# Performance work log

Hardware: AMD Instinct MI355X
Metric: run time of the kernel (lower is better)

Reference implementation:

```python
import jax, jax.numpy as jnp
import numpy as np

N_NODES = 65536
N_EDGES = 1048576


def gcn_conv(x, W, b, src, dst, n_nodes):
    """PyG GCNConv (normalize=True, add_self_loops already applied in src/dst):
    out = D^{-1/2} (A+I) D^{-1/2} X W + b, aggregated at dst (target) nodes."""
    deg = jax.ops.segment_sum(jnp.ones_like(dst, dtype=x.dtype), dst, num_segments=n_nodes)
    dis = jax.lax.rsqrt(jnp.maximum(deg, 1.0))  # self loops guarantee deg >= 1
    norm = dis[src] * dis[dst]                  # [E]
    h = x @ W                                   # [N, out]
    agg = jax.ops.segment_sum(h[src] * norm[:, None], dst, num_segments=n_nodes)
    return agg + b


def setup_inputs() -> dict:
    key = jax.random.key(0)
    ks = jax.random.split(key, 8)
    x = jax.random.normal(ks[0], (N_NODES, 128), dtype=jnp.float32)
    edge_index = jax.random.randint(ks[1], (2, N_EDGES), 0, N_NODES, dtype=jnp.int64)
    dims = [(128, 256), (256, 128), (128, 64)]
    params = {}
    for i, (din, dout) in enumerate(dims):
        scale = 1.0 / np.sqrt(din)
        params[f"W{i+1}"] = jax.random.uniform(ks[2 + i], (din, dout), dtype=jnp.float32, minval=-scale, maxval=scale)
        params[f"b{i+1}"] = jnp.zeros((dout,), dtype=jnp.float32)
    return {"x": x, "edge_index": edge_index, **params}


def reference(x, edge_index, W1, b1, W2, b2, W3, b3):
    n = x.shape[0]
    loop = jnp.arange(n, dtype=edge_index.dtype)
    src = jnp.concatenate([edge_index[0], loop])  # add self loops
    dst = jnp.concatenate([edge_index[1], loop])
    for W, b in ((W1, b1), (W2, b2), (W3, b3)):
        x = gcn_conv(x, W, b, src, dst, n)
        x = jax.nn.softmax(jax.nn.relu(x), axis=1)  # ReLU then Softmax(dim=1) per layer
    return x
```

## Files before the change

### kernel.cpp

```cpp
#include <hip/hip_runtime.h>
#include <cstdint>
#include <cstddef>

#define N_NODES 65536
#define N_EDGES 1048576
#define E_TOT   (N_EDGES + N_NODES)
#define CAP     5120

using short8  = __attribute__((ext_vector_type(8))) short;
using floatx4 = __attribute__((ext_vector_type(4))) float;
using half8   = __attribute__((ext_vector_type(8))) _Float16;
using half4   = __attribute__((ext_vector_type(4))) _Float16;
typedef unsigned short ushort_t;

__device__ inline void split_bf16(float a, short& hi, short& lo) {
    unsigned u  = __float_as_uint(a);
    unsigned hr = (u + 0x7fffu + ((u >> 16) & 1u)) >> 16;
    float    hf = __uint_as_float(hr << 16);
    hi = (short)hr;
    float    lf = a - hf;
    lo = (short)(__float_as_uint(lf) >> 16);
}


__global__ __launch_bounds__(1024) void k_bucket(const int* __restrict__ src, const int* __restrict__ dst,
                                                 int* __restrict__ gcur, unsigned* __restrict__ pk) {
    __shared__ int cnt[256];
    __shared__ int cur[256];
    int tid = threadIdx.x;
    if (tid < 256) cnt[tid] = 0;
    __syncthreads();
    int base = blockIdx.x * 4096;
    #pragma unroll
    for (int j = 0; j < 4; ++j) {
        int d = __builtin_nontemporal_load(&dst[base + j * 1024 + tid]);
        atomicAdd(&cnt[d >> 8], 1);
    }
    __syncthreads();
    if (tid < 256) cur[tid] = CAP * tid + atomicAdd(&gcur[tid], cnt[tid]);
    __syncthreads();
    #pragma unroll
    for (int j = 0; j < 4; ++j) {
        int e = base + j * 1024 + tid;
        int d = __builtin_nontemporal_load(&dst[e]);
        int s = __builtin_nontemporal_load(&src[e]);
        int pos = atomicAdd(&cur[d >> 8], 1);
        pk[pos] = ((unsigned)s << 16) | (unsigned)d;
    }
}

__global__ __launch_bounds__(256) void k_boff(const int* __restrict__ gcur, int* __restrict__ boff,
                                              int* __restrict__ off) {
    __shared__ int sb[256];
    int tid = threadIdx.x;
    int v = gcur[tid] + 256;
    sb[tid] = v;
    __syncthreads();
    #pragma unroll
    for (int s = 1; s < 256; s <<= 1) {
        int t = (tid >= s) ? sb[tid - s] : 0;
        __syncthreads();
        sb[tid] += t;
        __syncthreads();
    }
    boff[tid] = sb[tid] - v;
    if (tid == 255) boff[256] = sb[255];
    if (tid == 0) off[N_NODES] = E_TOT;
}

__global__ __launch_bounds__(1024) void k_sortb(const unsigned* __restrict__ pk, const int* __restrict__ gcur,
                                                const int* __restrict__ boff, int* __restrict__ off,
                                                float* __restrict__ dis, ushort_t* __restrict__ ssort) {
    __shared__ int cnt[256];
    __shared__ int sb[256];
    __shared__ int cur[256];
    int b = blockIdx.x;
    int tid = threadIdx.x;
    int n = gcur[b];
    const unsigned* p = pk + (size_t)b * CAP;
    if (tid < 256) cnt[tid] = 0;
    __syncthreads();
    for (int i = tid; i < n; i += 1024) atomicAdd(&cnt[p[i] & 255u], 1);
    __syncthreads();
    if (tid < 256) sb[tid] = cnt[tid];
    __syncthreads();
    #pragma unroll
    for (int s = 1; s < 256; s <<= 1) {
        int t = (tid < 256 && tid >= s) ? sb[tid - s] : 0;
        __syncthreads();
        if (tid < 256) sb[tid] += t;
        __syncthreads();
    }
    if (tid < 256) {
        int deg = cnt[tid];
        int o = boff[b] + (sb[tid] - deg) + tid;
        int d = b * 256 + tid;
        off[d] = o;
        dis[d] = rsqrtf((float)(deg + 1));
        ssort[o + deg] = (ushort_t)d;
        cur[tid] = o;
    }
    __syncthreads();
    for (int i = tid; i < n; i += 1024) {
        unsigned v = p[i];
        int pos = atomicAdd(&cur[v & 255u], 1);
        ssort[pos] = (ushort_t)(v >> 16);
    }
}


#define G1 (16 * 4 * 64)
#define G2 (8 * 8 * 64)
#define G3 (4 * 4 * 64)
#define NBX 8192
#define NBW ((G1 + G2 + G3 + 255) / 256)

__device__ inline void convw_split(const float* W, int K, int N, short* Bh, short* Bl, int g) {
    int lane = g & 63;
    int kt = (g >> 6) % (K / 32);
    int nt = (g >> 6) / (K / 32);
    int n = nt * 16 + (lane & 15);
    int kbase = kt * 32 + (lane >> 4) * 8;
    #pragma unroll
    for (int j = 0; j < 8; ++j) {
        short h, l;
        split_bf16(W[(size_t)(kbase + j) * N + n], h, l);
        Bh[(size_t)g * 8 + j] = h;
        Bl[(size_t)g * 8 + j] = l;
    }
}

__device__ inline void convw_h(const float* W, int K, int N, _Float16* Bf, int g) {
    int lane = g & 63;
    int kt = (g >> 6) % (K / 32);
    int nt = (g >> 6) / (K / 32);
    int n = nt * 16 + (lane & 15);
    int kbase = kt * 32 + (lane >> 4) * 8;
    #pragma unroll
    for (int j = 0; j < 8; ++j)
        Bf[(size_t)g * 8 + j] = (_Float16)W[(size_t)(kbase + j) * N + n];
}

__global__ __launch_bounds__(256) void k_fused(
        const float* __restrict__ x, const float* __restrict__ dis, _Float16* __restrict__ xh,
        const float* __restrict__ W1, short* __restrict__ w1h, short* __restrict__ w1l,
        const float* __restrict__ W2, _Float16* __restrict__ w2f,
        const float* __restrict__ W3, _Float16* __restrict__ w3f) {
    int b = blockIdx.x;
    if (b < NBX) {
        int idx = (b * 256 + threadIdx.x) * 4;
        int row = idx >> 7;
        float d = dis[row];
        float4 v = *(const float4*)(x + idx);
        half4 o = {(_Float16)(d * v.x), (_Float16)(d * v.y), (_Float16)(d * v.z), (_Float16)(d * v.w)};
        *(half4*)(xh + idx) = o;
    } else {
        int g = (b - NBX) * 256 + threadIdx.x;
        if (g < G1)                 convw_split(W1, 128, 256, w1h, w1l, g);
        else if (g < G1 + G2)       convw_h(W2, 256, 128, w2f, g - G1);
        else if (g < G1 + G2 + G3)  convw_h(W3, 128, 64, w3f, g - G1 - G2);
    }
}


template <int K, int N>
__global__ __launch_bounds__(256) void k_mms(const _Float16* __restrict__ A,
                                             const short* __restrict__ Bh, const short* __restrict__ Bl,
                                             const float* __restrict__ bias, _Float16* __restrict__ Cout) {
    constexpr int NT = N / 16;
    constexpr int KT = K / 32;
    int tid = threadIdx.x;
    int wave = tid >> 6, lane = tid & 63;
    int quad = lane >> 4, col = lane & 15;
    size_t row0 = (size_t)blockIdx.x * 64;
    const _Float16* ap = A + (row0 + wave * 16 + col) * K + quad * 8;

    floatx4 acc[NT];
    #pragma unroll
    for (int t = 0; t < NT; ++t) acc[t] = (floatx4)0.0f;

    for (int kt = 0; kt < KT; ++kt) {
        half8 a8 = *(const half8*)(ap + kt * 32);
        short ah[8], al[8];
        #pragma unroll
        for (int j = 0; j < 8; ++j) split_bf16((float)a8[j], ah[j], al[j]);
        short8 afh = *(short8*)ah;
        short8 afl = *(short8*)al;
        #pragma unroll
        for (int nt = 0; nt < NT; ++nt) {
            size_t bi = ((size_t)(nt * KT + kt) * 64 + lane);
            short8 bfh = ((const short8*)Bh)[bi];
            short8 bfl = ((const short8*)Bl)[bi];
            acc[nt] = __builtin_amdgcn_mfma_f32_16x16x32_bf16(afh, bfh, acc[nt], 0, 0, 0);
            acc[nt] = __builtin_amdgcn_mfma_f32_16x16x32_bf16(afh, bfl, acc[nt], 0, 0, 0);
            acc[nt] = __builtin_amdgcn_mfma_f32_16x16x32_bf16(afl, bfh, acc[nt], 0, 0, 0);
        }
    }

    size_t rbase = row0 + wave * 16 + quad * 4;
    float bv[NT];
    #pragma unroll
    for (int nt = 0; nt < NT; ++nt) bv[nt] = bias[nt * 16 + col];
    float mr[4] = {0.f, 0.f, 0.f, 0.f};
    #pragma unroll
    for (int nt = 0; nt < NT; ++nt)
        #pragma unroll
        for (int r = 0; r < 4; ++r) {
            float v = fmaxf(acc[nt][r] + bv[nt], 0.0f);
            acc[nt][r] = v;
            mr[r] = fmaxf(mr[r], v);
        }
    #pragma unroll
    for (int mask = 1; mask < 16; mask <<= 1)
        #pragma unroll
        for (int r = 0; r < 4; ++r) mr[r] = fmaxf(mr[r], __shfl_xor(mr[r], mask, 64));
    float sr[4] = {0.f, 0.f, 0.f, 0.f};
    #pragma unroll
    for (int nt = 0; nt < NT; ++nt)
        #pragma unroll
        for (int r = 0; r < 4; ++r) {
            float t = __expf(acc[nt][r] - mr[r]);
            acc[nt][r] = t;
            sr[r] += t;
        }
    #pragma unroll
    for (int mask = 1; mask < 16; mask <<= 1)
        #pragma unroll
        for (int r = 0; r < 4; ++r) sr[r] += __shfl_xor(sr[r], mask, 64);
    float inv[4];
    #pragma unroll
    for (int r = 0; r < 4; ++r) inv[r] = 1.0f / sr[r];
    #pragma unroll
    for (int nt = 0; nt < NT; ++nt)
        #pragma unroll
        for (int r = 0; r < 4; ++r)
            Cout[(rbase + r) * N + nt * 16 + col] = (_Float16)(acc[nt][r] * inv[r]);
}


template <int K, int N>
__global__ __launch_bounds__(256) void k_mmh(const _Float16* __restrict__ A,
                                             const _Float16* __restrict__ Bf,
                                             const float* __restrict__ dis, _Float16* __restrict__ Cout) {
    constexpr int NT = N / 16;
    constexpr int KT = K / 32;
    int tid = threadIdx.x;
    int wave = tid >> 6, lane = tid & 63;
    int quad = lane >> 4, col = lane & 15;
    size_t row0 = (size_t)blockIdx.x * 64;
    const _Float16* ap = A + (row0 + wave * 16 + col) * K + quad * 8;

    floatx4 acc[NT];
    #pragma unroll
    for (int t = 0; t < NT; ++t) acc[t] = (floatx4)0.0f;

    for (int kt = 0; kt < KT; ++kt) {
        half8 a8 = *(const half8*)(ap + kt * 32);
        #pragma unroll
        for (int nt = 0; nt < NT; ++nt) {
            half8 bf = ((const half8*)Bf)[(size_t)(nt * KT + kt) * 64 + lane];
            acc[nt] = __builtin_amdgcn_mfma_f32_16x16x32_f16(a8, bf, acc[nt], 0, 0, 0);
        }
    }

    size_t rbase = row0 + wave * 16 + quad * 4;
    float4 d4 = *(const float4*)(dis + rbase);
    float dr[4] = {d4.x, d4.y, d4.z, d4.w};
    #pragma unroll
    for (int nt = 0; nt < NT; ++nt)
        #pragma unroll
        for (int r = 0; r < 4; ++r)
            Cout[(rbase + r) * N + nt * 16 + col] = (_Float16)(acc[nt][r] * dr[r]);
}


template <bool ACT>
__global__ __launch_bounds__(256) void k_agg128h(const _Float16* __restrict__ h, const int* __restrict__ off,
                                                 const ushort_t* __restrict__ ss, const float* __restrict__ dis,
                                                 const float* __restrict__ bias, _Float16* __restrict__ out) {
    int lane = threadIdx.x & 63;
    int sub = lane >> 4;
    int li  = lane & 15;
    int c0  = li * 8;
    int n = blockIdx.x * 4 + (threadIdx.x >> 6);
    int e0 = off[n], e1 = off[n + 1];
    int e = e0;
    float acc[8];
    #pragma unroll
    for (int j = 0; j < 8; ++j) acc[j] = 0.0f;

    if (ACT) {
        half8 hacc = {0, 0, 0, 0, 0, 0, 0, 0};
        for (; e + 16 <= e1; e += 16) {
            int s0 = ss[e + sub];
            int s1 = ss[e + 4 + sub];
            int s2 = ss[e + 8 + sub];
            int s3 = ss[e + 12 + sub];
            half8 v0 = *(const half8*)(h + (size_t)s0 * 128 + c0);
            half8 v1 = *(const half8*)(h + (size_t)s1 * 128 + c0);
            half8 v2 = *(const half8*)(h + (size_t)s2 * 128 + c0);
            half8 v3 = *(const half8*)(h + (size_t)s3 * 128 + c0);
            hacc += (v0 + v1) + (v2 + v3);
        }
        for (; e + 8 <= e1; e += 8) {
            int sa = ss[e + sub];
            int sb = ss[e + 4 + sub];
            half8 va = *(const half8*)(h + (size_t)sa * 128 + c0);
            half8 vb = *(const half8*)(h + (size_t)sb * 128 + c0);
            hacc += va + vb;
        }
        #pragma unroll
        for (int j = 0; j < 8; ++j) acc[j] = (float)hacc[j];
    } else {
        for (; e + 16 <= e1; e += 16) {
            int s0 = ss[e + sub];
            int s1 = ss[e + 4 + sub];
            int s2 = ss[e + 8 + sub];
            int s3 = ss[e + 12 + sub];
            half8 v0 = *(const half8*)(h + (size_t)s0 * 128 + c0);
            half8 v1 = *(const half8*)(h + (size_t)s1 * 128 + c0);
            half8 v2 = *(const half8*)(h + (size_t)s2 * 128 + c0);
            half8 v3 = *(const half8*)(h + (size_t)s3 * 128 + c0);
            half8 vs = (v0 + v1) + (v2 + v3);
            #pragma unroll
            for (int j = 0; j < 8; ++j) acc[j] += (float)vs[j];
        }
        for (; e + 8 <= e1; e += 8) {
            int sa = ss[e + sub];
            int sb = ss[e + 4 + sub];
            half8 va = *(const half8*)(h + (size_t)sa * 128 + c0);
            half8 vb = *(const half8*)(h + (size_t)sb * 128 + c0);
            half8 vs = va + vb;
            #pragma unroll
            for (int j = 0; j < 8; ++j) acc[j] += (float)vs[j];
        }
    }
    while (e < e1) {
        int rem = e1 - e;
        int idx = e + sub;
        if (idx >= e1) idx = e1 - 1;
        int s = ss[idx];
        half8 v = *(const half8*)(h + (size_t)s * 128 + c0);
        float w = (sub < rem) ? 1.0f : 0.0f;
        #pragma unroll
        for (int j = 0; j < 8; ++j) acc[j] = fmaf(w, (float)v[j], acc[j]);
        e += 4;
    }

    #pragma unroll
    for (int mask = 32; mask >= 16; mask >>= 1)
        #pragma unroll
        for (int j = 0; j < 8; ++j) acc[j] += __shfl_xor(acc[j], mask, 64);

    float dn = dis[n];
    if (ACT) {
        float m = 0.0f;
        #pragma unroll
        for (int j = 0; j < 8; ++j) {
            float v = fmaxf(fmaf(acc[j], dn, bias[c0 + j]), 0.0f);
            acc[j] = v;
            m = fmaxf(m, v);
        }
        #pragma unroll
        for (int mask = 8; mask > 0; mask >>= 1) m = fmaxf(m, __shfl_xor(m, mask, 64));
        float sum = 0.0f;
        #pragma unroll
        for (int j = 0; j < 8; ++j) {
            float t = __expf(acc[j] - m);
            acc[j] = t;
            sum += t;
        }
        #pragma unroll
        for (int mask = 8; mask > 0; mask >>= 1) sum += __shfl_xor(sum, mask, 64);
        float inv = 1.0f / sum;
        #pragma unroll
        for (int j = 0; j < 8; ++j) acc[j] *= inv;
    } else {
        #pragma unroll
        for (int j = 0; j < 8; ++j) acc[j] *= dn;
    }
    if (sub == 0) {
        half8 o;
        #pragma unroll
        for (int j = 0; j < 8; ++j) o[j] = (_Float16)acc[j];
        *(half8*)(out + (size_t)n * 128 + c0) = o;
    }
}


__global__ __launch_bounds__(256) void k_agg64h(const _Float16* __restrict__ h, const int* __restrict__ off,
                                                const ushort_t* __restrict__ ss, const float* __restrict__ dis,
                                                const float* __restrict__ bias, float* __restrict__ out) {
    int lane = threadIdx.x & 63;
    int sub = lane >> 3;
    int li  = lane & 7;
    int c0  = li * 8;
    int n = blockIdx.x * 4 + (threadIdx.x >> 6);
    int e0 = off[n], e1 = off[n + 1];
    int e = e0;
    float acc[8];
    #pragma unroll
    for (int j = 0; j < 8; ++j) acc[j] = 0.0f;

    half8 hacc = {0, 0, 0, 0, 0, 0, 0, 0};
    for (; e + 16 <= e1; e += 16) {
        int s0 = ss[e + sub];
        int s1 = ss[e + 8 + sub];
        half8 v0 = *(const half8*)(h + (size_t)s0 * 64 + c0);
        half8 v1 = *(const half8*)(h + (size_t)s1 * 64 + c0);
        hacc += v0 + v1;
    }
    for (; e + 8 <= e1; e += 8) {
        int s = ss[e + sub];
        half8 v = *(const half8*)(h + (size_t)s * 64 + c0);
        hacc += v;
    }
    #pragma unroll
    for (int j = 0; j < 8; ++j) acc[j] = (float)hacc[j];

    int rem = e1 - e;
    if (rem > 0) {
        int idx = e + sub;
        if (idx >= e1) idx = e1 - 1;
        int s = ss[idx];
        half8 v = *(const half8*)(h + (size_t)s * 64 + c0);
        float w = (sub < rem) ? 1.0f : 0.0f;
        #pragma unroll
        for (int j = 0; j < 8; ++j) acc[j] = fmaf(w, (float)v[j], acc[j]);
    }

    #pragma unroll
    for (int mask = 32; mask >= 8; mask >>= 1)
        #pragma unroll
        for (int j = 0; j < 8; ++j) acc[j] += __shfl_xor(acc[j], mask, 64);

    float dn = dis[n];
    float m = 0.0f;
    #pragma unroll
    for (int j = 0; j < 8; ++j) {
        float v = fmaxf(fmaf(acc[j], dn, bias[c0 + j]), 0.0f);
        acc[j] = v;
        m = fmaxf(m, v);
    }
    #pragma unroll
    for (int mask = 4; mask > 0; mask >>= 1) m = fmaxf(m, __shfl_xor(m, mask, 64));
    float sum = 0.0f;
    #pragma unroll
    for (int j = 0; j < 8; ++j) {
        float t = __expf(acc[j] - m);
        acc[j] = t;
        sum += t;
    }
    #pragma unroll
    for (int mask = 4; mask > 0; mask >>= 1) sum += __shfl_xor(sum, mask, 64);
    float inv = 1.0f / sum;
    if (sub == 0) {
        float* op = out + (size_t)n * 64 + c0;
        *(float4*)(op)     = make_float4(acc[0] * inv, acc[1] * inv, acc[2] * inv, acc[3] * inv);
        *(float4*)(op + 4) = make_float4(acc[4] * inv, acc[5] * inv, acc[6] * inv, acc[7] * inv);
    }
}


extern "C" void kernel_launch(void* const* d_in, const int* in_sizes, int n_in,
                              void* d_out, int out_size, void* d_ws, size_t ws_size,
                              hipStream_t stream) {
    const float* x  = (const float*)d_in[0];
    const int*   ei = (const int*)d_in[1];
    const float* W1 = (const float*)d_in[2];
    const float* b1 = (const float*)d_in[3];
    const float* W2 = (const float*)d_in[4];
    const float* b2 = (const float*)d_in[5];
    const float* W3 = (const float*)d_in[6];
    const float* b3 = (const float*)d_in[7];
    const int* srcE = ei;
    const int* dstE = ei + N_EDGES;

    char* p = (char*)d_ws;
    auto carve = [&](size_t bytes) {
        char* q = p;
        p += (bytes + 255) & ~(size_t)255;
        return q;
    };
    int*          gcur  = (int*)carve(sizeof(int) * 256);
    int*          boff  = (int*)carve(sizeof(int) * 257);
    int*          off   = (int*)carve(sizeof(int) * (N_NODES + 1));
    float*        dis   = (float*)carve(sizeof(float) * N_NODES);
    unsigned*     pk    = (unsigned*)carve(sizeof(unsigned) * 256 * CAP);
    ushort_t*     ssort = (ushort_t*)carve(sizeof(ushort_t) * E_TOT);
    short*        w1h   = (short*)carve(sizeof(short) * 128 * 256);
    short*        w1l   = (short*)carve(sizeof(short) * 128 * 256);
    _Float16*     w2f   = (_Float16*)carve(sizeof(_Float16) * 256 * 128);
    _Float16*     w3f   = (_Float16*)carve(sizeof(_Float16) * 128 * 64);
    _Float16*     xh    = (_Float16*)carve(sizeof(_Float16) * (size_t)N_NODES * 128);
    _Float16*     a0h   = (_Float16*)carve(sizeof(_Float16) * (size_t)N_NODES * 128);
    _Float16*     x1h   = (_Float16*)carve(sizeof(_Float16) * (size_t)N_NODES * 256);
    _Float16*     x2h   = (_Float16*)carve(sizeof(_Float16) * (size_t)N_NODES * 128);
    _Float16*     hh    = (_Float16*)carve(sizeof(_Float16) * (size_t)N_NODES * 128);

    (void)hipMemsetAsync(gcur, 0, sizeof(int) * 256, stream);
    k_bucket<<<256, 1024, 0, stream>>>(srcE, dstE, gcur, pk);
    k_boff<<<1, 256, 0, stream>>>(gcur, boff, off);
    k_sortb<<<256, 1024, 0, stream>>>(pk, gcur, boff, off, dis, ssort);
    k_fused<<<NBX + NBW, 256, 0, stream>>>(x, dis, xh, W1, w1h, w1l, W2, w2f, W3, w3f);

    k_agg128h<false><<<N_NODES / 4, 256, 0, stream>>>(xh, off, ssort, dis, nullptr, a0h);
    k_mms<128, 256><<<N_NODES / 64, 256, 0, stream>>>(a0h, w1h, w1l, b1, x1h);
    k_mmh<256, 128><<<N_NODES / 64, 256, 0, stream>>>(x1h, w2f, dis, hh);
    k_agg128h<true><<<N_NODES / 4, 256, 0, stream>>>(hh, off, ssort, dis, b2, x2h);
    k_mmh<128, 64><<<N_NODES / 64, 256, 0, stream>>>(x2h, w3f, dis, hh);
    k_agg64h<<<N_NODES / 4, 256, 0, stream>>>(hh, off, ssort, dis, b3, (float*)d_out);
}
```

Measured before the change: 292.8 us.

## Assign multiple nodes per wavefront in aggregation kernels instead of one

```diff
diff --git a/kernel.cpp b/kernel.cpp
--- a/kernel.cpp
+++ b/kernel.cpp
@@ -274,190 +274,105 @@
 }
 
 
-template <bool ACT>
-__global__ __launch_bounds__(256) void k_agg128h(const _Float16* __restrict__ h, const int* __restrict__ off,
-                                                 const ushort_t* __restrict__ ss, const float* __restrict__ dis,
-                                                 const float* __restrict__ bias, _Float16* __restrict__ out) {
+template <int LPN, bool ACT, typename OutT>
+__global__ __launch_bounds__(256) void k_aggq(const _Float16* __restrict__ h, const int* __restrict__ off,
+                                              const ushort_t* __restrict__ ss, const float* __restrict__ dis,
+                                              const float* __restrict__ bias, OutT* __restrict__ out) {
+    constexpr int D = LPN * 8;
+    constexpr int NPW = 64 / LPN;
     int lane = threadIdx.x & 63;
-    int sub = lane >> 4;
-    int li  = lane & 15;
-    int c0  = li * 8;
-    int n = blockIdx.x * 4 + (threadIdx.x >> 6);
+    int grp  = lane / LPN;
+    int li   = lane & (LPN - 1);
+    int c0   = li * 8;
+    int n = (blockIdx.x * 4 + (threadIdx.x >> 6)) * NPW + grp;
     int e0 = off[n], e1 = off[n + 1];
+
+    const _Float16* hb = h + c0;
+
+    half8 hacc = {0, 0, 0, 0, 0, 0, 0, 0};
+    float facc[8];
+    #pragma unroll
+    for (int j = 0; j < 8; ++j) facc[j] = 0.0f;
+
     int e = e0;
-    float acc[8];
-    #pragma unroll
-    for (int j = 0; j < 8; ++j) acc[j] = 0.0f;
-
-    if (ACT) {
-        half8 hacc = {0, 0, 0, 0, 0, 0, 0, 0};
-        for (; e + 16 <= e1; e += 16) {
-            int s0 = ss[e + sub];
-            int s1 = ss[e + 4 + sub];
-            int s2 = ss[e + 8 + sub];
-            int s3 = ss[e + 12 + sub];
-            half8 v0 = *(const half8*)(h + (size_t)s0 * 128 + c0);
-            half8 v1 = *(const half8*)(h + (size_t)s1 * 128 + c0);
-            half8 v2 = *(const half8*)(h + (size_t)s2 * 128 + c0);
-            half8 v3 = *(const half8*)(h + (size_t)s3 * 128 + c0);
-            hacc += (v0 + v1) + (v2 + v3);
-        }
-        for (; e + 8 <= e1; e += 8) {
-            int sa = ss[e + sub];
-            int sb = ss[e + 4 + sub];
-            half8 va = *(const half8*)(h + (size_t)sa * 128 + c0);
-            half8 vb = *(const half8*)(h + (size_t)sb * 128 + c0);
-            hacc += va + vb;
-        }
-        #pragma unroll
-        for (int j = 0; j < 8; ++j) acc[j] = (float)hacc[j];
-    } else {
-        for (; e + 16 <= e1; e += 16) {
-            int s0 = ss[e + sub];
-            int s1 = ss[e + 4 + sub];
-            int s2 = ss[e + 8 + sub];
-            int s3 = ss[e + 12 + sub];
-            half8 v0 = *(const half8*)(h + (size_t)s0 * 128 + c0);
-            half8 v1 = *(const half8*)(h + (size_t)s1 * 128 + c0);
-            half8 v2 = *(const half8*)(h + (size_t)s2 * 128 + c0);
-            half8 v3 = *(const half8*)(h + (size_t)s3 * 128 + c0);
-            half8 vs = (v0 + v1) + (v2 + v3);
+    for (; e + 4 <= e1; e += 4) {
+        int s0 = ss[e];
+        int s1 = ss[e + 1];
+        int s2 = ss[e + 2];
+        int s3 = ss[e + 3];
+        half8 v0 = *(const half8*)(hb + (size_t)s0 * D);
+        half8 v1 = *(const half8*)(hb + (size_t)s1 * D);
+        half8 v2 = *(const half8*)(hb + (size_t)s2 * D);
+        half8 v3 = *(const half8*)(hb + (size_t)s3 * D);
+        half8 p = (v0 + v1) + (v2 + v3);
+        if constexpr (ACT) {
+            hacc += p;
+        } else {
             #pragma unroll
-            for (int j = 0; j < 8; ++j) acc[j] += (float)vs[j];
-        }
-        for (; e + 8 <= e1; e += 8) {
-            int sa = ss[e + sub];
-            int sb = ss[e + 4 + sub];
-            half8 va = *(const half8*)(h + (size_t)sa * 128 + c0);
-            half8 vb = *(const half8*)(h + (size_t)sb * 128 + c0);
-            half8 vs = va + vb;
-            #pragma unroll
-            for (int j = 0; j < 8; ++j) acc[j] += (float)vs[j];
-        }
-    }
-    while (e < e1) {
-        int rem = e1 - e;
-        int idx = e + sub;
-        if (idx >= e1) idx = e1 - 1;
-        int s = ss[idx];
-        half8 v = *(const half8*)(h + (size_t)s * 128 + c0);
-        float w = (sub < rem) ? 1.0f : 0.0f;
-        #pragma unroll
-        for (int j = 0; j < 8; ++j) acc[j] = fmaf(w, (float)v[j], acc[j]);
-        e += 4;
-    }
-
-    #pragma unroll
-    for (int mask = 32; mask >= 16; mask >>= 1)
-        #pragma unroll
-        for (int j = 0; j < 8; ++j) acc[j] += __shfl_xor(acc[j], mask, 64);
-
-    float dn = dis[n];
-    if (ACT) {
-        float m = 0.0f;
-        #pragma unroll
-        for (int j = 0; j < 8; ++j) {
-            float v = fmaxf(fmaf(acc[j], dn, bias[c0 + j]), 0.0f);
-            acc[j] = v;
-            m = fmaxf(m, v);
-        }
-        #pragma unroll
-        for (int mask = 8; mask > 0; mask >>= 1) m = fmaxf(m, __shfl_xor(m, mask, 64));
-        float sum = 0.0f;
-        #pragma unroll
-        for (int j = 0; j < 8; ++j) {
-            float t = __expf(acc[j] - m);
-            acc[j] = t;
-            sum += t;
-        }
-        #pragma unroll
-        for (int mask = 8; mask > 0; mask >>= 1) sum += __shfl_xor(sum, mask, 64);
-        float inv = 1.0f / sum;
-        #pragma unroll
-        for (int j = 0; j < 8; ++j) acc[j] *= inv;
-    } else {
-        #pragma unroll
-        for (int j = 0; j < 8; ++j) acc[j] *= dn;
-    }
-    if (sub == 0) {
-        half8 o;
-        #pragma unroll
-        for (int j = 0; j < 8; ++j) o[j] = (_Float16)acc[j];
-        *(half8*)(out + (size_t)n * 128 + c0) = o;
-    }
-}
-
-
-__global__ __launch_bounds__(256) void k_agg64h(const _Float16* __restrict__ h, const int* __restrict__ off,
-                                                const ushort_t* __restrict__ ss, const float* __restrict__ dis,
-                                                const float* __restrict__ bias, float* __restrict__ out) {
-    int lane = threadIdx.x & 63;
-    int sub = lane >> 3;
-    int li  = lane & 7;
-    int c0  = li * 8;
-    int n = blockIdx.x * 4 + (threadIdx.x >> 6);
-    int e0 = off[n], e1 = off[n + 1];
-    int e = e0;
-    float acc[8];
-    #pragma unroll
-    for (int j = 0; j < 8; ++j) acc[j] = 0.0f;
-
-    half8 hacc = {0, 0, 0, 0, 0, 0, 0, 0};
-    for (; e + 16 <= e1; e += 16) {
-        int s0 = ss[e + sub];
-        int s1 = ss[e + 8 + sub];
-        half8 v0 = *(const half8*)(h + (size_t)s0 * 64 + c0);
-        half8 v1 = *(const half8*)(h + (size_t)s1 * 64 + c0);
-        hacc += v0 + v1;
-    }
-    for (; e + 8 <= e1; e += 8) {
-        int s = ss[e + sub];
-        half8 v = *(const half8*)(h + (size_t)s * 64 + c0);
-        hacc += v;
-    }
-    #pragma unroll
-    for (int j = 0; j < 8; ++j) acc[j] = (float)hacc[j];
-
+            for (int j = 0; j < 8; ++j) facc[j] += (float)p[j];
+        }
+    }
     int rem = e1 - e;
     if (rem > 0) {
-        int idx = e + sub;
-        if (idx >= e1) idx = e1 - 1;
-        int s = ss[idx];
-        half8 v = *(const half8*)(h + (size_t)s * 64 + c0);
-        float w = (sub < rem) ? 1.0f : 0.0f;
-        #pragma unroll
-        for (int j = 0; j < 8; ++j) acc[j] = fmaf(w, (float)v[j], acc[j]);
-    }
-
-    #pragma unroll
-    for (int mask = 32; mask >= 8; mask >>= 1)
-        #pragma unroll
-        for (int j = 0; j < 8; ++j) acc[j] += __shfl_xor(acc[j], mask, 64);
+        int s0 = ss[e];
+        half8 p = *(const half8*)(hb + (size_t)s0 * D);
+        if (rem > 1) {
+            int s1 = ss[e + 1];
+            p += *(const half8*)(hb + (size_t)s1 * D);
+        }
+        if (rem > 2) {
+            int s2 = ss[e + 2];
+            p += *(const half8*)(hb + (size_t)s2 * D);
+        }
+        if constexpr (ACT) {
+            hacc += p;
+        } else {
+            #pragma unroll
+            for (int j = 0; j < 8; ++j) facc[j] += (float)p[j];
+        }
+    }
+    if constexpr (ACT) {
+        #pragma unroll
+        for (int j = 0; j < 8; ++j) facc[j] = (float)hacc[j];
+    }
 
     float dn = dis[n];
-    float m = 0.0f;
-    #pragma unroll
-    for (int j = 0; j < 8; ++j) {
-        float v = fmaxf(fmaf(acc[j], dn, bias[c0 + j]), 0.0f);
-        acc[j] = v;
-        m = fmaxf(m, v);
-    }
-    #pragma unroll
-    for (int mask = 4; mask > 0; mask >>= 1) m = fmaxf(m, __shfl_xor(m, mask, 64));
-    float sum = 0.0f;
-    #pragma unroll
-    for (int j = 0; j < 8; ++j) {
-        float t = __expf(acc[j] - m);
-        acc[j] = t;
-        sum += t;
-    }
-    #pragma unroll
-    for (int mask = 4; mask > 0; mask >>= 1) sum += __shfl_xor(sum, mask, 64);
-    float inv = 1.0f / sum;
-    if (sub == 0) {
-        float* op = out + (size_t)n * 64 + c0;
-        *(float4*)(op)     = make_float4(acc[0] * inv, acc[1] * inv, acc[2] * inv, acc[3] * inv);
-        *(float4*)(op + 4) = make_float4(acc[4] * inv, acc[5] * inv, acc[6] * inv, acc[7] * inv);
+    if constexpr (ACT) {
+        float m = 0.0f;
+        #pragma unroll
+        for (int j = 0; j < 8; ++j) {
+            float v = fmaxf(fmaf(facc[j], dn, bias[c0 + j]), 0.0f);
+            facc[j] = v;
+            m = fmaxf(m, v);
+        }
+        #pragma unroll
+        for (int mask = LPN / 2; mask > 0; mask >>= 1) m = fmaxf(m, __shfl_xor(m, mask, 64));
+        float sum = 0.0f;
+        #pragma unroll
+        for (int j = 0; j < 8; ++j) {
+            float t = __expf(facc[j] - m);
+            facc[j] = t;
+            sum += t;
+        }
+        #pragma unroll
+        for (int mask = LPN / 2; mask > 0; mask >>= 1) sum += __shfl_xor(sum, mask, 64);
+        float inv = 1.0f / sum;
+        #pragma unroll
+        for (int j = 0; j < 8; ++j) facc[j] *= inv;
+    } else {
+        #pragma unroll
+        for (int j = 0; j < 8; ++j) facc[j] *= dn;
+    }
+
+    if constexpr (sizeof(OutT) == 2) {
+        half8 o;
+        #pragma unroll
+        for (int j = 0; j < 8; ++j) o[j] = (_Float16)facc[j];
+        *(half8*)((_Float16*)out + (size_t)n * D + c0) = o;
+    } else {
+        float* op = (float*)out + (size_t)n * D + c0;
+        *(float4*)(op)     = make_float4(facc[0], facc[1], facc[2], facc[3]);
+        *(float4*)(op + 4) = make_float4(facc[4], facc[5], facc[6], facc[7]);
     }
 }
 
@@ -504,10 +419,10 @@
     k_sortb<<<256, 1024, 0, stream>>>(pk, gcur, boff, off, dis, ssort);
     k_fused<<<NBX + NBW, 256, 0, stream>>>(x, dis, xh, W1, w1h, w1l, W2, w2f, W3, w3f);
 
-    k_agg128h<false><<<N_NODES / 4, 256, 0, stream>>>(xh, off, ssort, dis, nullptr, a0h);
+    k_aggq<16, false, _Float16><<<N_NODES / 16, 256, 0, stream>>>(xh, off, ssort, dis, nullptr, a0h);
     k_mms<128, 256><<<N_NODES / 64, 256, 0, stream>>>(a0h, w1h, w1l, b1, x1h);
     k_mmh<256, 128><<<N_NODES / 64, 256, 0, stream>>>(x1h, w2f, dis, hh);
-    k_agg128h<true><<<N_NODES / 4, 256, 0, stream>>>(hh, off, ssort, dis, b2, x2h);
+    k_aggq<16, true, _Float16><<<N_NODES / 16, 256, 0, stream>>>(hh, off, ssort, dis, b2, x2h);
     k_mmh<128, 64><<<N_NODES / 64, 256, 0, stream>>>(x2h, w3f, dis, hh);
-    k_agg64h<<<N_NODES / 4, 256, 0, stream>>>(hh, off, ssort, dis, b3, (float*)d_out);
-}
+    k_aggq<8, true, float><<<N_NODES / 32, 256, 0, stream>>>(hh, off, ssort, dis, b3, (float*)d_out);
+}
```

Result: faster. 278.3 us (-5.0%).
